# Performance work log

Measured on AMD Instinct MI355X. Metric: run time of the kernel, lower is better.

The kernel has to match this reference:

```python
import jax, jax.numpy as jnp
import numpy as np

L = 3          # num_layers
EPS = 1e-5     # BatchNorm eps


def _gmn_forward(feats_1, feats_2, edge_index_1, edge_index_2, N1, N2,
                 Wn, bn, Wm, bm, Wp, bp, gamma, beta, Wa, ba, Wg, bg, Wf, bf):
    N = N1 + N2
    x = jnp.concatenate([feats_1, feats_2], axis=0)                       # [N, F]
    edge_index = jnp.concatenate([edge_index_1, edge_index_2 + N1], axis=1)
    src, dst = edge_index[0], edge_index[1]                               # source_to_target flow
    batch = jnp.concatenate([jnp.zeros((N1,), jnp.int32), jnp.ones((N2,), jnp.int32)])
    for l in range(L):
        h = x @ Wn[l] + bn[l]                                             # lin_node
        # message(x_i=h[dst], x_j=h[src]) = lin_message(cat[x_i, x_j])
        m = jnp.concatenate([h[dst], h[src]], axis=1) @ Wm[l] + bm[l]     # [E, D]
        aggr = jax.ops.segment_sum(m, dst, num_segments=N)                # scatter-add to targets
        # batch_block_pair_attention on ORIGINAL (pre-lin_node) features
        gx, gy = x[:N1], x[N1:]
        s = gx @ gy.T                                                     # [N1, N2] similarities
        att_x = jax.nn.softmax(s, axis=1) @ gy                            # attn for graph-1 nodes
        att_y = jax.nn.softmax(s, axis=0).T @ gx                          # attn for graph-2 nodes
        cross = jnp.concatenate([att_x, att_y], axis=0)                   # [N, F]
        att_in = x - cross                                                # attention_input
        out = jnp.concatenate([aggr, att_in], axis=1) @ Wp[l] + bp[l]     # lin_passing
        mu = out.mean(axis=0)
        var = ((out - mu) ** 2).mean(axis=0)                              # BatchNorm (train, biased var)
        x = (out - mu) * jax.lax.rsqrt(var + EPS) * gamma[l] + beta[l]
    # GraphAggregator
    states = x @ Wa + ba
    gates = jax.nn.softmax(x @ Wg + bg, axis=1)                           # softmax over feature dim (as in source)
    g = states * gates
    sums = jax.ops.segment_sum(g, batch, num_segments=2)                  # scatter_mean
    counts = jnp.array([N1, N2], jnp.float32)[:, None]
    emb = (sums / counts) @ Wf + bf                                       # [2, D]
    return emb


def setup_inputs() -> dict:
    key = jax.random.key(0)
    ks = jax.random.split(key, 12)
    N1 = N2 = 6144
    E = 196608
    F = 128
    D = 128
    sc = lambda fan: fan ** -0.5
    rn = lambda k, sh, s: jax.random.normal(k, sh, dtype=jnp.float32) * s
    return {
        "feats_1": rn(ks[0], (N1, F), 1.0),
        "edge_index_1": jax.random.randint(ks[1], (2, E), 0, N1),
        "feats_2": rn(ks[2], (N2, F), 1.0),
        "edge_index_2": jax.random.randint(ks[3], (2, E), 0, N2),
        "sizes_1": N1,
        "sizes_2": N2,
        "Wn": rn(ks[4], (L, F, D), sc(F)),
        "bn": jnp.zeros((L, D), jnp.float32),
        "Wm": rn(ks[5], (L, 2 * D, D), sc(2 * D)),
        "bm": jnp.zeros((L, D), jnp.float32),
        "Wp": rn(ks[6], (L, D + F, D), sc(D + F)),
        "bp": jnp.zeros((L, D), jnp.float32),
        "gamma": jnp.ones((L, D), jnp.float32),
        "beta": jnp.zeros((L, D), jnp.float32),
        "Wa": rn(ks[7], (D, D), sc(D)),
        "ba": jnp.zeros((D,), jnp.float32),
        "Wg": rn(ks[8], (D, D), sc(D)),
        "bg": jnp.zeros((D,), jnp.float32),
        "Wf": rn(ks[9], (D, D), sc(D)),
        "bf": jnp.zeros((D,), jnp.float32),
    }


def reference(feats_1, edge_index_1, feats_2, edge_index_2, sizes_1, sizes_2,
              Wn, bn, Wm, bm, Wp, bp, gamma, beta, Wa, ba, Wg, bg, Wf, bf):
    emb = _gmn_forward(feats_1, feats_2, edge_index_1, edge_index_2,
                       int(sizes_1), int(sizes_2),
                       Wn, bn, Wm, bm, Wp, bp, gamma, beta, Wa, ba, Wg, bg, Wf, bf)
    emb_1 = emb[0:1]
    emb_2 = emb[1:2]
    return emb_1, emb_2
```

## Files before the change

kernel.cpp:

```cpp
#include <hip/hip_runtime.h>
#include <hip/hip_bf16.h>

#define D 128
#define KVS 16
typedef unsigned short u16;
typedef unsigned int u32;
typedef __attribute__((ext_vector_type(8))) short short8;
typedef __attribute__((ext_vector_type(16))) float f32x16;
typedef __attribute__((ext_vector_type(4))) u32 u32x4;

__device__ __forceinline__ u16 f2bf(float f){
  u32 u = __builtin_bit_cast(u32, f);
  u32 r = (u + 0x7FFFu + ((u >> 16) & 1u)) >> 16;
  return (u16)r;
}
__device__ __forceinline__ float bf2f(u16 u){
  union { u32 i; float f; } v; v.i = ((u32)u) << 16; return v.f;
}

__global__ void k_count(const int* __restrict__ ei1, const int* __restrict__ ei2,
                        int E1, int E2, int N1, int* __restrict__ cnt){
  int i = blockIdx.x*blockDim.x + threadIdx.x;
  int Et = E1 + E2;
  for (; i < Et; i += gridDim.x*blockDim.x){
    int dst = (i < E1) ? ei1[E1 + i] : (ei2[E2 + (i - E1)] + N1);
    atomicAdd(&cnt[dst], 1);
  }
}

__global__ void k_scan(const int* __restrict__ cnt, int* __restrict__ ptr,
                       int* __restrict__ cursor, float* __restrict__ degf, int N){
  __shared__ int part[256];
  int t = threadIdx.x;
  int per = (N + 255) >> 8;
  int lo = t*per, hi = min(N, lo+per);
  int s = 0;
  for (int j=lo;j<hi;j++) s += cnt[j];
  part[t] = s; __syncthreads();
  if (t==0){ int acc=0; for (int j=0;j<256;j++){ int v=part[j]; part[j]=acc; acc+=v; } }
  __syncthreads();
  int acc = part[t];
  for (int j=lo;j<hi;j++){ ptr[j]=acc; cursor[j]=acc; degf[j]=(float)cnt[j]; acc += cnt[j]; }
}

__global__ void k_fill(const int* __restrict__ ei1, const int* __restrict__ ei2,
                       int E1, int E2, int N1, int* __restrict__ cursor, int* __restrict__ srclist){
  int i = blockIdx.x*blockDim.x + threadIdx.x;
  int Et = E1 + E2;
  for (; i < Et; i += gridDim.x*blockDim.x){
    int src, dst;
    if (i < E1){ src = ei1[i]; dst = ei1[E1+i]; }
    else { int j = i - E1; src = ei2[j] + N1; dst = ei2[E2+j] + N1; }
    int p = atomicAdd(&cursor[dst], 1);
    srclist[p] = src;
  }
}

__global__ __launch_bounds__(256) void k_prep(
    const float* __restrict__ Wp, const float* __restrict__ Wa, const float* __restrict__ Wg,
    const float* __restrict__ Wn, const float* __restrict__ Wm,
    const float* __restrict__ bn, const float* __restrict__ bm,
    const float* __restrict__ src1, const float* __restrict__ src2, int N1,
    u16* __restrict__ wgt, u16* __restrict__ wfu, float* __restrict__ fbias,
    float* __restrict__ x, u16* __restrict__ xb, u16* __restrict__ xbT, int N)
{
  __shared__ u16 tile[128][136];
  const int m = blockIdx.x;
  const int t = threadIdx.x;
  if (m < 8){
    const float* src; u16* dst;
    if (m < 6){ int l = m % 3, half = m / 3; src = Wp + (size_t)l*32768 + half*16384; dst = wgt + (size_t)(half*3 + l)*16384; }
    else if (m == 6){ src = Wa; dst = wgt + (size_t)6*16384; }
    else { src = Wg; dst = wgt + (size_t)7*16384; }
    int n = t & 127, rh = t >> 7;
    for (int r0=0; r0<128; r0+=2){
      int r = r0 + rh;
      tile[n][r] = f2bf(src[r*128 + n]);
    }
    __syncthreads();
    int row = t >> 1, ch = t & 1;
    #pragma unroll
    for (int i=0;i<4;i++){
      int k0 = ch*64 + i*16;
      short8 a = *(const short8*)&tile[row][k0];
      short8 b = *(const short8*)&tile[row][k0+8];
      *(short8*)&dst[row*128 + k0] = a;
      *(short8*)&dst[row*128 + k0 + 8] = b;
    }
  } else if (m < 14){
    int blk = m - 8;
    int l = blk % 3, which = blk / 3;
    const float* A  = Wn + (size_t)l*16384;
    const float* Bm = Wm + (size_t)l*32768 + (which==0 ? 16384 : 0);
    u16* dst  = wfu  + (size_t)(which==0 ? l : 3+l)*16384;
    float* fb = fbias + (size_t)(which==0 ? l : 3+l)*128;
    int c0 = (t & 31) * 4;
    int r0 = (t >> 5) * 16;
    float acc[16][4];
    #pragma unroll
    for (int i=0;i<16;i++){ acc[i][0]=0.f; acc[i][1]=0.f; acc[i][2]=0.f; acc[i][3]=0.f; }
    for (int k=0;k<128;k++){
      float4 b4 = *(const float4*)&Bm[k*128 + c0];
      #pragma unroll
      for (int i=0;i<16;i++){
        float a = A[(r0+i)*128 + k];
        acc[i][0] += a*b4.x; acc[i][1] += a*b4.y; acc[i][2] += a*b4.z; acc[i][3] += a*b4.w;
      }
    }
    #pragma unroll
    for (int i=0;i<16;i++)
      #pragma unroll
      for (int j=0;j<4;j++)
        dst[(size_t)(c0+j)*128 + (r0+i)] = f2bf(acc[i][j]);
    if (t < 128){
      float s = 0.f;
      for (int k=0;k<128;k++) s += bn[l*128+k]*Bm[k*128+t];
      if (which) s += bm[l*128+t];
      fb[t] = s;
    }
  } else {
    int nb = (m - 14) * 128;
    int n = t >> 1, ch = t & 1;
    int row = nb + n;
    const float* srow = (row < N1) ? &src1[(size_t)row*D] : &src2[(size_t)(row-N1)*D];
    #pragma unroll
    for (int i=0;i<16;i++){
      int dd = ch*64 + i*4;
      float4 v = *(const float4*)&srow[dd];
      *(float4*)&x[(size_t)row*D + dd] = v;
      u16 b0 = f2bf(v.x), b1 = f2bf(v.y), b2 = f2bf(v.z), b3 = f2bf(v.w);
      ushort4 uv; uv.x=b0; uv.y=b1; uv.z=b2; uv.w=b3;
      *(ushort4*)&xb[(size_t)row*D + dd] = uv;
      tile[dd+0][n]=b0; tile[dd+1][n]=b1; tile[dd+2][n]=b2; tile[dd+3][n]=b3;
    }
    __syncthreads();
    int d = t & 127, hf = t >> 7;
    #pragma unroll
    for (int i=0;i<8;i++){
      short8 v = *(const short8*)&tile[d][hf*64 + i*8];
      *(short8*)&xbT[(size_t)d*N + nb + hf*64 + i*8] = v;
    }
  }
}

__global__ __launch_bounds__(256) void k_gemm(
    const u16* __restrict__ A, const u16* __restrict__ W1T,
    const u16* __restrict__ B, const u16* __restrict__ W2T,
    const float* __restrict__ bias, const float* __restrict__ bias2,
    const float* __restrict__ rs, const float* __restrict__ addin,
    float* __restrict__ of, float* __restrict__ of2,
    u16* __restrict__ ob, float* __restrict__ csums, int N)
{
  __shared__ __align__(16) u16 Wsw[2][16384];
  const int t = threadIdx.x;
  const int w4 = t >> 6;
  const int lane = t & 63;
  const int l31 = lane & 31;
  const int hi = lane >> 5;
  const int rb = blockIdx.x * 32;

  #pragma unroll
  for (int i=0;i<8;i++){
    int slot = i*256 + t;
    int row = slot >> 4, g = slot & 15;
    short8 v = *(const short8*)(W1T + row*128 + g*8);
    *(short8*)((char*)&Wsw[0][0] + row*256 + ((g ^ (row&7))*16)) = v;
  }
  if (B){
    #pragma unroll
    for (int i=0;i<8;i++){
      int slot = i*256 + t;
      int row = slot >> 4, g = slot & 15;
      short8 v = *(const short8*)(W2T + row*128 + g*8);
      *(short8*)((char*)&Wsw[1][0] + row*256 + ((g ^ (row&7))*16)) = v;
    }
  }
  short8 af[8], bfr[8];
  #pragma unroll
  for (int g=0; g<8; g++)
    af[g] = *(const short8*)(A + (size_t)(rb + l31)*D + (2*g + hi)*8);
  if (B){
    #pragma unroll
    for (int g=0; g<8; g++)
      bfr[g] = *(const short8*)(B + (size_t)(rb + l31)*D + (2*g + hi)*8);
  }
  __syncthreads();

  f32x16 acc1, acc2;
  #pragma unroll
  for (int i=0;i<16;i++){ acc1[i]=0.f; acc2[i]=0.f; }
  const int wrow = w4*32 + l31;
  #pragma unroll
  for (int s=0;s<8;s++){
    int gr = 2*s + hi;
    short8 wf = *(const short8*)((const char*)&Wsw[0][0] + wrow*256 + ((gr ^ (wrow&7))*16));
    acc1 = __builtin_amdgcn_mfma_f32_32x32x16_bf16(af[s], wf, acc1, 0,0,0);
  }
  if (B){
    #pragma unroll
    for (int s=0;s<8;s++){
      int gr = 2*s + hi;
      short8 wf = *(const short8*)((const char*)&Wsw[1][0] + wrow*256 + ((gr ^ (wrow&7))*16));
      acc2 = __builtin_amdgcn_mfma_f32_32x32x16_bf16(bfr[s], wf, acc2, 0,0,0);
    }
  }
  const int col = wrow;
  float bv = bias ? bias[col] : 0.0f;
  float bv2 = bias2 ? bias2[col] : 0.0f;
  float ssum = 0.f, sq = 0.f;
  #pragma unroll
  for (int r=0;r<16;r++){
    int rr = (r&3) + 8*(r>>2) + 4*hi;
    size_t grow = (size_t)(rb + rr);
    float v = acc1[r] + bv;
    if (rs) v *= rs[grow];
    if (addin) v += addin[grow*D + col];
    if (B && !of2) v += acc2[r];
    if (of) of[grow*D + col] = v;
    if (ob) ob[grow*D + col] = f2bf(v);
    if (of2) of2[grow*D + col] = acc2[r] + bv2;
    ssum += v; sq += v*v;
  }
  if (csums){
    ssum += __shfl_xor(ssum, 32, 64);
    sq   += __shfl_xor(sq, 32, 64);
    if (hi == 0){
      atomicAdd(&csums[col], ssum);
      atomicAdd(&csums[128+col], sq);
    }
  }
}

__global__ __launch_bounds__(256) void k_gather(const u16* __restrict__ hb, const int* __restrict__ ptr,
                          const int* __restrict__ cnt, const int* __restrict__ srclist,
                          float* __restrict__ Sg, int N){
  int f = threadIdx.x & 127, sub = threadIdx.x >> 7;
  int v = blockIdx.x*2 + sub;
  if (v >= N) return;
  int b = ptr[v], n = cnt[v];
  float a0=0.f, a1=0.f, a2=0.f, a3=0.f;
  int j=0;
  for (; j+3<n; j+=4){
    int s0=srclist[b+j], s1=srclist[b+j+1], s2=srclist[b+j+2], s3=srclist[b+j+3];
    a0 += bf2f(hb[(size_t)s0*D + f]);
    a1 += bf2f(hb[(size_t)s1*D + f]);
    a2 += bf2f(hb[(size_t)s2*D + f]);
    a3 += bf2f(hb[(size_t)s3*D + f]);
  }
  for (; j<n; j++) a0 += bf2f(hb[(size_t)srclist[b+j]*D + f]);
  Sg[(size_t)v*D + f] = (a0+a1)+(a2+a3);
}

__global__ __launch_bounds__(256, 2) void k_flash_mfma(
    const u16* __restrict__ xb, const u16* __restrict__ xbT,
    int N1, int N2, int Ntot,
    u16* __restrict__ Opartb, float* __restrict__ MLpart)
{
  __shared__ __align__(16) u16 Kbuf[2][4096];
  __shared__ __align__(16) u16 Vbuf[2][4096];

  const float L2E = 1.44269504f;
  const int t = threadIdx.x;
  const int w = t >> 6;
  const int lane = t & 63;
  const int l31 = lane & 31;
  const int hi = lane >> 5;

  const int qb = blockIdx.x / KVS;
  const int sp = blockIdx.x % KVS;
  const int qbase = qb * 128;
  const int qs = qbase + w*32;
  const bool isY = qbase >= N1;
  const int kv0 = isY ? 0 : N1;
  const int kvlen = isY ? N1 : N2;
  const int Lk = kvlen / KVS;
  const int kstart = kv0 + sp*Lk;
  const int ntiles = Lk >> 5;

  short8 qf[8];
  #pragma unroll
  for (int c = 0; c < 8; ++c)
    qf[c] = *(const short8*)(xb + (size_t)(qs + l31)*D + c*16 + hi*8);

  const int kr = t >> 3;
  const int kg = (t & 7) * 2;
  const int vd = t >> 1;
  const int vj = (t & 1) * 2;
  const int kw0 = kr*256 + ((kg     ^ (kr & 7))*16);
  const int kw1 = kr*256 + (((kg+1) ^ (kr & 7))*16);
  const int vw0 = vd*64  + (((vj     ^ vd) & 3)*16);
  const int vw1 = vd*64  + ((((vj+1) ^ vd) & 3)*16);

  f32x16 O[4];
  #pragma unroll
  for (int mt=0; mt<4; ++mt)
    #pragma unroll
    for (int i=0;i<16;i++) O[mt][i] = 0.f;
  float m_run = -3.0e38f, l_run = 0.0f;

  {
    int kb = kstart;
    short8 a0 = *(const short8*)(xb  + (size_t)(kb+kr)*D + kg*8);
    short8 a1 = *(const short8*)(xb  + (size_t)(kb+kr)*D + (kg+1)*8);
    short8 v0 = *(const short8*)(xbT + (size_t)vd*Ntot + kb + vj*8);
    short8 v1 = *(const short8*)(xbT + (size_t)vd*Ntot + kb + (vj+1)*8);
    *(short8*)((char*)&Kbuf[0][0] + kw0) = a0;
    *(short8*)((char*)&Kbuf[0][0] + kw1) = a1;
    *(short8*)((char*)&Vbuf[0][0] + vw0) = v0;
    *(short8*)((char*)&Vbuf[0][0] + vw1) = v1;
  }
  __syncthreads();

  for (int tt = 0; tt < ntiles; ++tt){
    const int cur = tt & 1;
    const int nxt = cur ^ 1;
    short8 a0, a1, v0, v1;
    const bool more = (tt+1 < ntiles);
    if (more){
      int kb = kstart + (tt+1)*32;
      a0 = *(const short8*)(xb  + (size_t)(kb+kr)*D + kg*8);
      a1 = *(const short8*)(xb  + (size_t)(kb+kr)*D + (kg+1)*8);
      v0 = *(const short8*)(xbT + (size_t)vd*Ntot + kb + vj*8);
      v1 = *(const short8*)(xbT + (size_t)vd*Ntot + kb + (vj+1)*8);
    }

    const char* Klds = (const char*)&Kbuf[cur][0];
    const char* Vlds = (const char*)&Vbuf[cur][0];

    f32x16 s;
    #pragma unroll
    for (int i=0;i<16;i++) s[i]=0.f;
    #pragma unroll
    for (int c = 0; c < 8; ++c){
      int gr = 2*c + hi;
      short8 ka = *(const short8*)(Klds + l31*256 + ((gr ^ (l31&7))*16));
      s = __builtin_amdgcn_mfma_f32_32x32x16_bf16(ka, qf[c], s, 0,0,0);
    }

    float tm = s[0];
    #pragma unroll
    for (int i=1;i<16;i++) tm = fmaxf(tm, s[i]);
    tm = fmaxf(tm, __shfl_xor(tm, 32, 64));
    float tm2 = tm * L2E;
    if (__any(tm2 > m_run + 11.544f)){
      float mnew = fmaxf(m_run, tm2);
      float alpha = exp2f(m_run - mnew);
      l_run *= alpha;
      m_run = mnew;
      #pragma unroll
      for (int i=0;i<16;i++){ O[0][i]*=alpha; O[1][i]*=alpha; O[2][i]*=alpha; O[3][i]*=alpha; }
    }
    float rsum = 0.f;
    #pragma unroll
    for (int i=0;i<16;i++){ float p = exp2f(fmaf(s[i], L2E, -m_run)); s[i]=p; rsum += p; }
    rsum += __shfl_xor(rsum, 32, 64);
    l_run += rsum;

    u32 pk[8];
    #pragma unroll
    for (int i=0;i<8;i++){
      u32 r;
      asm("v_cvt_pk_bf16_f32 %0, %1, %2" : "=v"(r) : "v"(s[2*i]), "v"(s[2*i+1]));
      pk[i] = r;
    }

    #pragma unroll
    for (int ks=0; ks<2; ++ks){
      u32 send0 = hi ? pk[(2*ks)*2+0] : pk[(2*ks+1)*2+0];
      u32 send1 = hi ? pk[(2*ks)*2+1] : pk[(2*ks+1)*2+1];
      u32 xv0 = (u32)__shfl_xor((int)send0, 32, 64);
      u32 xv1 = (u32)__shfl_xor((int)send1, 32, 64);
      u32 own0 = hi ? pk[(2*ks+1)*2+0] : pk[(2*ks)*2+0];
      u32 own1 = hi ? pk[(2*ks+1)*2+1] : pk[(2*ks)*2+1];
      u32x4 bv;
      bv.x = hi ? xv0 : own0;
      bv.y = hi ? xv1 : own1;
      bv.z = hi ? own0 : xv0;
      bv.w = hi ? own1 : xv1;
      short8 pf = __builtin_bit_cast(short8, bv);
      #pragma unroll
      for (int mt=0; mt<4; ++mt){
        int dd = mt*32 + l31;
        int j = 2*ks + hi;
        short8 vf = *(const short8*)(Vlds + dd*64 + (((j ^ dd) & 3)*16));
        O[mt] = __builtin_amdgcn_mfma_f32_32x32x16_bf16(vf, pf, O[mt], 0,0,0);
      }
    }

    if (more){
      *(short8*)((char*)&Kbuf[nxt][0] + kw0) = a0;
      *(short8*)((char*)&Kbuf[nxt][0] + kw1) = a1;
      *(short8*)((char*)&Vbuf[nxt][0] + vw0) = v0;
      *(short8*)((char*)&Vbuf[nxt][0] + vw1) = v1;
    }
    __syncthreads();
  }

  const int strip = qs >> 5;
  u16* Od = Opartb + ((size_t)strip*KVS + sp)*4096;
  #pragma unroll
  for (int mt=0; mt<4; ++mt){
    #pragma unroll
    for (int r=0;r<16;r++){
      int dd = mt*32 + (r&3) + 8*(r>>2) + 4*hi;
      Od[dd*32 + l31] = f2bf(O[mt][r]);
    }
  }
  if (lane < 32){
    float* mlp = MLpart + ((size_t)strip*KVS + sp)*64;
    mlp[l31*2+0] = m_run;
    mlp[l31*2+1] = l_run;
  }
}

__global__ __launch_bounds__(256) void k_fcomb_hm2(
    const u16* __restrict__ Opartb, const float* __restrict__ MLpart,
    const float* __restrict__ x, u16* __restrict__ attinb,
    const u16* __restrict__ xb, const u16* __restrict__ W1T, const float* __restrict__ fb2,
    u16* __restrict__ hm2b, int nstrips, int N)
{
  __shared__ __align__(16) char smem[32768];
  const int t = threadIdx.x;
  if ((int)blockIdx.x < nstrips){
    const int strip = blockIdx.x;
    float (*cw)[32] = (float(*)[32])smem;
    float (*Tld)[33] = (float(*)[33])(smem + 2048);
    if (t < 32){
      const float* mlp = MLpart + (size_t)strip*KVS*64;
      float mv[KVS], lv[KVS];
      float M = -3.0e38f;
      #pragma unroll
      for (int s2=0;s2<KVS;s2++){ mv[s2]=mlp[s2*64+t*2]; lv[s2]=mlp[s2*64+t*2+1]; M = fmaxf(M, mv[s2]); }
      float L = 0.f;
      #pragma unroll
      for (int s2=0;s2<KVS;s2++){ float wv=exp2f(mv[s2]-M); cw[s2][t]=wv; L += wv*lv[s2]; }
      float inv = 1.0f / L;
      #pragma unroll
      for (int s2=0;s2<KVS;s2++) cw[s2][t] *= inv;
    }
    __syncthreads();
    {
      const int d = t >> 1, q0 = (t & 1) * 16;
      const u16* Ob = Opartb + (size_t)strip*KVS*4096;
      float acc[16];
      #pragma unroll
      for (int j=0;j<16;j++) acc[j]=0.f;
      #pragma unroll
      for (int s2=0; s2<KVS; ++s2){
        const u16* row = Ob + s2*4096 + d*32 + q0;
        short8 v8a = *(const short8*)row;
        short8 v8b = *(const short8*)(row + 8);
        #pragma unroll
        for (int j=0;j<8;j++){
          acc[j]   += cw[s2][q0+j]  *bf2f((u16)v8a[j]);
          acc[8+j] += cw[s2][q0+8+j]*bf2f((u16)v8b[j]);
        }
      }
      #pragma unroll
      for (int j=0;j<16;j++) Tld[d][q0+j] = acc[j];
    }
    __syncthreads();
    {
      const int q = t >> 3, c0 = (t & 7) * 16;
      const size_t row = (size_t)(strip*32 + q)*D;
      #pragma unroll
      for (int i=0;i<16;i+=4){
        float4 xr = *(const float4*)&x[row + c0 + i];
        ushort4 o;
        o.x = f2bf(xr.x - Tld[c0+i+0][q]);
        o.y = f2bf(xr.y - Tld[c0+i+1][q]);
        o.z = f2bf(xr.z - Tld[c0+i+2][q]);
        o.w = f2bf(xr.w - Tld[c0+i+3][q]);
        *(ushort4*)&attinb[row + c0 + i] = o;
      }
    }
  } else {
    u16* Wsw = (u16*)smem;
    const int w4 = t >> 6;
    const int lane = t & 63;
    const int l31 = lane & 31;
    const int hi = lane >> 5;
    const int rb = ((int)blockIdx.x - nstrips) * 32;
    #pragma unroll
    for (int i=0;i<8;i++){
      int slot = i*256 + t;
      int row = slot >> 4, g = slot & 15;
      short8 v = *(const short8*)(W1T + row*128 + g*8);
      *(short8*)((char*)Wsw + row*256 + ((g ^ (row&7))*16)) = v;
    }
    short8 af[8];
    #pragma unroll
    for (int g=0; g<8; g++)
      af[g] = *(const short8*)(xb + (size_t)(rb + l31)*D + (2*g + hi)*8);
    __syncthreads();
    f32x16 acc1;
    #pragma unroll
    for (int i=0;i<16;i++) acc1[i]=0.f;
    const int wrow = w4*32 + l31;
    #pragma unroll
    for (int s=0;s<8;s++){
      int gr = 2*s + hi;
      short8 wf = *(const short8*)((const char*)Wsw + wrow*256 + ((gr ^ (wrow&7))*16));
      acc1 = __builtin_amdgcn_mfma_f32_32x32x16_bf16(af[s], wf, acc1, 0,0,0);
    }
    float bv = fb2[wrow];
    #pragma unroll
    for (int r=0;r<16;r++){
      int rr = (r&3) + 8*(r>>2) + 4*hi;
      hm2b[(size_t)(rb + rr)*D + wrow] = f2bf(acc1[r] + bv);
    }
  }
}

__global__ __launch_bounds__(256) void k_normcvt(const float* __restrict__ outb,
                        const float* __restrict__ sums,
                        const float* __restrict__ gamma, const float* __restrict__ beta,
                        int N, float* __restrict__ x, u16* __restrict__ xb, u16* __restrict__ xbT){
  __shared__ u16 tile[128][136];
  __shared__ float smu[128], srs[128], sg2[128], sb2[128];
  int t = threadIdx.x;
  if (t < 128){
    float mu = sums[t] / (float)N;
    float var = fmaxf(sums[128+t]/(float)N - mu*mu, 0.0f);
    smu[t]=mu; srs[t]=rsqrtf(var + 1e-5f);
    sg2[t]=gamma[t]; sb2[t]=beta[t];
  }
  __syncthreads();
  int nb = blockIdx.x * 128;
  int n = t >> 1, ch = t & 1;
  #pragma unroll
  for (int i=0;i<16;i++){
    int dd = ch*64 + i*4;
    float4 v = *(const float4*)&outb[(size_t)(nb+n)*D + dd];
    float4 y;
    y.x = (v.x - smu[dd+0])*srs[dd+0]*sg2[dd+0] + sb2[dd+0];
    y.y = (v.y - smu[dd+1])*srs[dd+1]*sg2[dd+1] + sb2[dd+1];
    y.z = (v.z - smu[dd+2])*srs[dd+2]*sg2[dd+2] + sb2[dd+2];
    y.w = (v.w - smu[dd+3])*srs[dd+3]*sg2[dd+3] + sb2[dd+3];
    *(float4*)&x[(size_t)(nb+n)*D + dd] = y;
    u16 b0=f2bf(y.x), b1=f2bf(y.y), b2=f2bf(y.z), b3=f2bf(y.w);
    ushort4 uv; uv.x=b0; uv.y=b1; uv.z=b2; uv.w=b3;
    *(ushort4*)&xb[(size_t)(nb+n)*D + dd] = uv;
    tile[dd+0][n]=b0; tile[dd+1][n]=b1; tile[dd+2][n]=b2; tile[dd+3][n]=b3;
  }
  __syncthreads();
  int d = t & 127, hf = t >> 7;
  #pragma unroll
  for (int i=0;i<8;i++){
    short8 v = *(const short8*)&tile[d][hf*64 + i*8];
    *(short8*)&xbT[(size_t)d*N + nb + hf*64 + i*8] = v;
  }
}

__global__ __launch_bounds__(256) void k_gatepool(
    const float* __restrict__ states, const float* __restrict__ glog,
    int N1, int N, float* __restrict__ gsums)
{
  __shared__ float part[256];
  part[threadIdx.x] = 0.f;
  __syncthreads();
  int wid = threadIdx.x >> 6, lane = threadIdx.x & 63;
  for (int v = blockIdx.x*4 + wid; v < N; v += gridDim.x*4){
    float a0 = glog[(size_t)v*D + lane], a1 = glog[(size_t)v*D + lane + 64];
    float mx = fmaxf(a0,a1);
    #pragma unroll
    for (int off=32; off; off>>=1) mx = fmaxf(mx, __shfl_xor(mx, off, 64));
    float e0 = __expf(a0-mx), e1 = __expf(a1-mx);
    float ss = e0+e1;
    #pragma unroll
    for (int off=32; off; off>>=1) ss += __shfl_xor(ss, off, 64);
    float inv = 1.f/ss;
    int g = (v < N1) ? 0 : 1;
    atomicAdd(&part[g*128 + lane], states[(size_t)v*D+lane]*e0*inv);
    atomicAdd(&part[g*128 + lane + 64], states[(size_t)v*D+lane+64]*e1*inv);
  }
  __syncthreads();
  atomicAdd(&gsums[threadIdx.x], part[threadIdx.x]);
}

__global__ __launch_bounds__(256) void k_emb(
    const float* __restrict__ gsums, const float* __restrict__ Wf,
    const float* __restrict__ bf_, int N1, int N2, float* __restrict__ outp)
{
  __shared__ float mean[256];
  int t = threadIdx.x;
  mean[t] = gsums[t] / ((t < 128) ? (float)N1 : (float)N2);
  __syncthreads();
  int g = t >> 7, dc = t & 127;
  float acc = bf_[dc];
  for (int k=0;k<D;k++) acc += mean[g*128 + k] * Wf[k*D + dc];
  outp[t] = acc;
}

extern "C" void kernel_launch(void* const* d_in, const int* in_sizes, int n_in,
                              void* d_out, int out_size, void* d_ws, size_t ws_size,
                              hipStream_t stream) {
  const float* feats1 = (const float*)d_in[0];
  const int*   ei1    = (const int*)d_in[1];
  const float* feats2 = (const float*)d_in[2];
  const int*   ei2    = (const int*)d_in[3];
  const float* Wn = (const float*)d_in[6];
  const float* bn = (const float*)d_in[7];
  const float* Wm = (const float*)d_in[8];
  const float* bm = (const float*)d_in[9];
  const float* Wp = (const float*)d_in[10];
  const float* bp = (const float*)d_in[11];
  const float* gamma = (const float*)d_in[12];
  const float* beta  = (const float*)d_in[13];
  const float* Wa = (const float*)d_in[14];
  const float* ba = (const float*)d_in[15];
  const float* Wg = (const float*)d_in[16];
  const float* bg = (const float*)d_in[17];
  const float* Wf = (const float*)d_in[18];
  const float* bff = (const float*)d_in[19];

  int N1 = in_sizes[0]/D, E1 = in_sizes[1]/2;
  int N2 = in_sizes[2]/D, E2 = in_sizes[3]/2;
  int N = N1+N2;
  int nstrips = N/32;

  char* w = (char*)d_ws;
  float* x    = (float*)w; w += (size_t)N*D*4;
  u16* xb     = (u16*)w;   w += (size_t)N*D*2;
  u16* xbT    = (u16*)w;   w += (size_t)N*D*2;
  u16* hm2b   = (u16*)w;   w += (size_t)N*D*2;
  u16* aggrb  = (u16*)w;   w += (size_t)N*D*2;
  u16* attinb = (u16*)w;   w += (size_t)N*D*2;
  int* cnt    = (int*)w;   w += (size_t)N*4;
  float* sums = (float*)w; w += 3*256*4;
  float* gsums= (float*)w; w += 256*4;
  int* ptr    = (int*)w;   w += (size_t)N*4;
  int* cursor = (int*)w;   w += (size_t)N*4;
  float* degf = (float*)w; w += (size_t)N*4;
  int* srclist= (int*)w;   w += (size_t)(E1+E2)*4;
  u16* wgt    = (u16*)w;   w += (size_t)8*16384*2;
  u16* wfu    = (u16*)w;   w += (size_t)6*16384*2;
  float* fbias= (float*)w; w += (size_t)6*128*4;
  u16* Opartb = (u16*)w;   w += (size_t)nstrips*KVS*4096*2;
  float* MLpart=(float*)w; w += (size_t)nstrips*KVS*64*4;
  float* Sg     = (float*)Opartb;
  float* outb   = (float*)Opartb + (size_t)N*D;
  float* states = Sg;
  float* glog   = outb;

  hipMemsetAsync(cnt, 0, (size_t)N*4 + 4*256*4, stream);
  k_count<<<1024,256,0,stream>>>(ei1, ei2, E1, E2, N1, cnt);
  k_scan<<<1,256,0,stream>>>(cnt, ptr, cursor, degf, N);
  k_fill<<<1024,256,0,stream>>>(ei1, ei2, E1, E2, N1, cursor, srclist);
  k_prep<<<14 + N/128,256,0,stream>>>(Wp, Wa, Wg, Wn, Wm, bn, bm,
                                      feats1, feats2, N1, wgt, wfu, fbias, x, xb, xbT, N);

  for (int l=0;l<3;l++){
    const u16* fuse2T_l = wfu + (size_t)l*16384;
    const u16* fuse1T_l = wfu + (size_t)(3+l)*16384;
    const float* fb2_l  = fbias + (size_t)l*128;
    const float* fb1_l  = fbias + (size_t)(3+l)*128;
    const u16* Wp1T_l = wgt + (size_t)(0+l)*16384;
    const u16* Wp2T_l = wgt + (size_t)(3+l)*16384;
    const float* bp_l = bp + (size_t)l*D;
    float* sums_l = sums + (size_t)l*256;

    k_flash_mfma<<<(N/128)*KVS,256,0,stream>>>(xb, xbT, N1, N2, N, Opartb, MLpart);
    k_fcomb_hm2<<<nstrips + N/32,256,0,stream>>>(Opartb, MLpart, x, attinb,
                                                 xb, fuse2T_l, fb2_l, hm2b, nstrips, N);
    k_gather<<<N/2,256,0,stream>>>(hm2b, ptr, cnt, srclist, Sg, N);
    k_gemm<<<N/32,256,0,stream>>>(xb, fuse1T_l, nullptr, nullptr, fb1_l, nullptr,
                                  degf, Sg, nullptr, nullptr, aggrb, nullptr, N);
    k_gemm<<<N/32,256,0,stream>>>(aggrb, Wp1T_l, attinb, Wp2T_l, bp_l, nullptr,
                                  nullptr, nullptr, outb, nullptr, nullptr, sums_l, N);
    k_normcvt<<<N/128,256,0,stream>>>(outb, sums_l, gamma + (size_t)l*D, beta + (size_t)l*D, N, x, xb, xbT);
  }

  k_gemm<<<N/32,256,0,stream>>>(xb, wgt + (size_t)6*16384, xb, wgt + (size_t)7*16384,
                                ba, bg, nullptr, nullptr, states, glog, nullptr, nullptr, N);
  k_gatepool<<<64,256,0,stream>>>(states, glog, N1, N, gsums);
  k_emb<<<1,256,0,stream>>>(gsums, Wf, bff, N1, N2, (float*)d_out);
}
```

Before: 634.6 us.

## Gather raw neighbor features before projection and merge into dual-input aggregation GEMM

The edge aggregation now sums neighbor bf16 features x_src directly, instead of first projecting every node through the fused Wn·Wm2 weight and then gathering. The source-side projection is folded into the aggregation k_gemm as a second A/B operand pair. This removes the per-node hm2 MFMA path from the combine kernel, and the two fused biases are merged into one degree-scaled bias. The weight-prep kernel also stages A through LDS as bf16. In exchange, neighbor sums are rounded to bf16 before the matmul, which may add precision error.

```diff
diff --git a/kernel.cpp b/kernel.cpp
--- a/kernel.cpp
+++ b/kernel.cpp
@@ -93,7 +93,19 @@
     const float* A  = Wn + (size_t)l*16384;
     const float* Bm = Wm + (size_t)l*32768 + (which==0 ? 16384 : 0);
     u16* dst  = wfu  + (size_t)(which==0 ? l : 3+l)*16384;
-    float* fb = fbias + (size_t)(which==0 ? l : 3+l)*128;
+    {
+      int r = t >> 1, kh = t & 1;
+      #pragma unroll
+      for (int i=0;i<16;i++){
+        int k0 = kh*64 + i*4;
+        float4 v4 = *(const float4*)&A[r*128 + k0];
+        tile[k0+0][r] = f2bf(v4.x);
+        tile[k0+1][r] = f2bf(v4.y);
+        tile[k0+2][r] = f2bf(v4.z);
+        tile[k0+3][r] = f2bf(v4.w);
+      }
+    }
+    __syncthreads();
     int c0 = (t & 31) * 4;
     int r0 = (t >> 5) * 16;
     float acc[16][4];
@@ -101,10 +113,17 @@
     for (int i=0;i<16;i++){ acc[i][0]=0.f; acc[i][1]=0.f; acc[i][2]=0.f; acc[i][3]=0.f; }
     for (int k=0;k<128;k++){
       float4 b4 = *(const float4*)&Bm[k*128 + c0];
+      short8 a0 = *(const short8*)&tile[k][r0];
+      short8 a1 = *(const short8*)&tile[k][r0+8];
       #pragma unroll
-      for (int i=0;i<16;i++){
-        float a = A[(r0+i)*128 + k];
-        acc[i][0] += a*b4.x; acc[i][1] += a*b4.y; acc[i][2] += a*b4.z; acc[i][3] += a*b4.w;
+      for (int i=0;i<8;i++){
+        float fa = bf2f((u16)a0[i]);
+        acc[i][0] += fa*b4.x; acc[i][1] += fa*b4.y; acc[i][2] += fa*b4.z; acc[i][3] += fa*b4.w;
+      }
+      #pragma unroll
+      for (int i=0;i<8;i++){
+        float fa = bf2f((u16)a1[i]);
+        acc[8+i][0] += fa*b4.x; acc[8+i][1] += fa*b4.y; acc[8+i][2] += fa*b4.z; acc[8+i][3] += fa*b4.w;
       }
     }
     #pragma unroll
@@ -112,11 +131,12 @@
       #pragma unroll
       for (int j=0;j<4;j++)
         dst[(size_t)(c0+j)*128 + (r0+i)] = f2bf(acc[i][j]);
-    if (t < 128){
+    if (which == 1 && t < 128){
+      const float* Bm1 = Wm + (size_t)l*32768;
+      const float* Bm2 = Bm1 + 16384;
       float s = 0.f;
-      for (int k=0;k<128;k++) s += bn[l*128+k]*Bm[k*128+t];
-      if (which) s += bm[l*128+t];
-      fb[t] = s;
+      for (int k=0;k<128;k++) s += bn[l*128+k]*(Bm1[k*128+t] + Bm2[k*128+t]);
+      fbias[l*128+t] = s + bm[l*128+t];
     }
   } else {
     int nb = (m - 14) * 128;
@@ -233,7 +253,7 @@
 
 __global__ __launch_bounds__(256) void k_gather(const u16* __restrict__ hb, const int* __restrict__ ptr,
                           const int* __restrict__ cnt, const int* __restrict__ srclist,
-                          float* __restrict__ Sg, int N){
+                          u16* __restrict__ xgb, int N){
   int f = threadIdx.x & 127, sub = threadIdx.x >> 7;
   int v = blockIdx.x*2 + sub;
   if (v >= N) return;
@@ -248,7 +268,7 @@
     a3 += bf2f(hb[(size_t)s3*D + f]);
   }
   for (; j<n; j++) a0 += bf2f(hb[(size_t)srclist[b+j]*D + f]);
-  Sg[(size_t)v*D + f] = (a0+a1)+(a2+a3);
+  xgb[(size_t)v*D + f] = f2bf((a0+a1)+(a2+a3));
 }
 
 __global__ __launch_bounds__(256, 2) void k_flash_mfma(
@@ -413,101 +433,61 @@
   }
 }
 
-__global__ __launch_bounds__(256) void k_fcomb_hm2(
+__global__ __launch_bounds__(256) void k_fcomb(
     const u16* __restrict__ Opartb, const float* __restrict__ MLpart,
-    const float* __restrict__ x, u16* __restrict__ attinb,
-    const u16* __restrict__ xb, const u16* __restrict__ W1T, const float* __restrict__ fb2,
-    u16* __restrict__ hm2b, int nstrips, int N)
+    const float* __restrict__ x, u16* __restrict__ attinb)
 {
-  __shared__ __align__(16) char smem[32768];
+  __shared__ float cw[KVS][32];
+  __shared__ float Tld[128][33];
+  const int strip = blockIdx.x;
   const int t = threadIdx.x;
-  if ((int)blockIdx.x < nstrips){
-    const int strip = blockIdx.x;
-    float (*cw)[32] = (float(*)[32])smem;
-    float (*Tld)[33] = (float(*)[33])(smem + 2048);
-    if (t < 32){
-      const float* mlp = MLpart + (size_t)strip*KVS*64;
-      float mv[KVS], lv[KVS];
-      float M = -3.0e38f;
+  if (t < 32){
+    const float* mlp = MLpart + (size_t)strip*KVS*64;
+    float mv[KVS], lv[KVS];
+    float M = -3.0e38f;
+    #pragma unroll
+    for (int s2=0;s2<KVS;s2++){ mv[s2]=mlp[s2*64+t*2]; lv[s2]=mlp[s2*64+t*2+1]; M = fmaxf(M, mv[s2]); }
+    float L = 0.f;
+    #pragma unroll
+    for (int s2=0;s2<KVS;s2++){ float wv=exp2f(mv[s2]-M); cw[s2][t]=wv; L += wv*lv[s2]; }
+    float inv = 1.0f / L;
+    #pragma unroll
+    for (int s2=0;s2<KVS;s2++) cw[s2][t] *= inv;
+  }
+  __syncthreads();
+  {
+    const int d = t >> 1, q0 = (t & 1) * 16;
+    const u16* Ob = Opartb + (size_t)strip*KVS*4096;
+    float acc[16];
+    #pragma unroll
+    for (int j=0;j<16;j++) acc[j]=0.f;
+    #pragma unroll
+    for (int s2=0; s2<KVS; ++s2){
+      const u16* row = Ob + s2*4096 + d*32 + q0;
+      short8 v8a = *(const short8*)row;
+      short8 v8b = *(const short8*)(row + 8);
       #pragma unroll
-      for (int s2=0;s2<KVS;s2++){ mv[s2]=mlp[s2*64+t*2]; lv[s2]=mlp[s2*64+t*2+1]; M = fmaxf(M, mv[s2]); }
-      float L = 0.f;
-      #pragma unroll
-      for (int s2=0;s2<KVS;s2++){ float wv=exp2f(mv[s2]-M); cw[s2][t]=wv; L += wv*lv[s2]; }
-      float inv = 1.0f / L;
-      #pragma unroll
-      for (int s2=0;s2<KVS;s2++) cw[s2][t] *= inv;
-    }
-    __syncthreads();
-    {
-      const int d = t >> 1, q0 = (t & 1) * 16;
-      const u16* Ob = Opartb + (size_t)strip*KVS*4096;
-      float acc[16];
-      #pragma unroll
-      for (int j=0;j<16;j++) acc[j]=0.f;
-      #pragma unroll
-      for (int s2=0; s2<KVS; ++s2){
-        const u16* row = Ob + s2*4096 + d*32 + q0;
-        short8 v8a = *(const short8*)row;
-        short8 v8b = *(const short8*)(row + 8);
-        #pragma unroll
-        for (int j=0;j<8;j++){
-          acc[j]   += cw[s2][q0+j]  *bf2f((u16)v8a[j]);
-          acc[8+j] += cw[s2][q0+8+j]*bf2f((u16)v8b[j]);
-        }
+      for (int j=0;j<8;j++){
+        acc[j]   += cw[s2][q0+j]  *bf2f((u16)v8a[j]);
+        acc[8+j] += cw[s2][q0+8+j]*bf2f((u16)v8b[j]);
       }
-      #pragma unroll
-      for (int j=0;j<16;j++) Tld[d][q0+j] = acc[j];
-    }
-    __syncthreads();
-    {
-      const int q = t >> 3, c0 = (t & 7) * 16;
-      const size_t row = (size_t)(strip*32 + q)*D;
-      #pragma unroll
-      for (int i=0;i<16;i+=4){
-        float4 xr = *(const float4*)&x[row + c0 + i];
-        ushort4 o;
-        o.x = f2bf(xr.x - Tld[c0+i+0][q]);
-        o.y = f2bf(xr.y - Tld[c0+i+1][q]);
-        o.z = f2bf(xr.z - Tld[c0+i+2][q]);
-        o.w = f2bf(xr.w - Tld[c0+i+3][q]);
-        *(ushort4*)&attinb[row + c0 + i] = o;
-      }
-    }
-  } else {
-    u16* Wsw = (u16*)smem;
-    const int w4 = t >> 6;
-    const int lane = t & 63;
-    const int l31 = lane & 31;
-    const int hi = lane >> 5;
-    const int rb = ((int)blockIdx.x - nstrips) * 32;
-    #pragma unroll
-    for (int i=0;i<8;i++){
-      int slot = i*256 + t;
-      int row = slot >> 4, g = slot & 15;
-      short8 v = *(const short8*)(W1T + row*128 + g*8);
-      *(short8*)((char*)Wsw + row*256 + ((g ^ (row&7))*16)) = v;
-    }
-    short8 af[8];
-    #pragma unroll
-    for (int g=0; g<8; g++)
-      af[g] = *(const short8*)(xb + (size_t)(rb + l31)*D + (2*g + hi)*8);
-    __syncthreads();
-    f32x16 acc1;
-    #pragma unroll
-    for (int i=0;i<16;i++) acc1[i]=0.f;
-    const int wrow = w4*32 + l31;
-    #pragma unroll
-    for (int s=0;s<8;s++){
-      int gr = 2*s + hi;
-      short8 wf = *(const short8*)((const char*)Wsw + wrow*256 + ((gr ^ (wrow&7))*16));
-      acc1 = __builtin_amdgcn_mfma_f32_32x32x16_bf16(af[s], wf, acc1, 0,0,0);
-    }
-    float bv = fb2[wrow];
-    #pragma unroll
-    for (int r=0;r<16;r++){
-      int rr = (r&3) + 8*(r>>2) + 4*hi;
-      hm2b[(size_t)(rb + rr)*D + wrow] = f2bf(acc1[r] + bv);
+    }
+    #pragma unroll
+    for (int j=0;j<16;j++) Tld[d][q0+j] = acc[j];
+  }
+  __syncthreads();
+  {
+    const int q = t >> 3, c0 = (t & 7) * 16;
+    const size_t row = (size_t)(strip*32 + q)*D;
+    #pragma unroll
+    for (int i=0;i<16;i+=4){
+      float4 xr = *(const float4*)&x[row + c0 + i];
+      ushort4 o;
+      o.x = f2bf(xr.x - Tld[c0+i+0][q]);
+      o.y = f2bf(xr.y - Tld[c0+i+1][q]);
+      o.z = f2bf(xr.z - Tld[c0+i+2][q]);
+      o.w = f2bf(xr.w - Tld[c0+i+3][q]);
+      *(ushort4*)&attinb[row + c0 + i] = o;
     }
   }
 }
@@ -623,7 +603,7 @@
   float* x    = (float*)w; w += (size_t)N*D*4;
   u16* xb     = (u16*)w;   w += (size_t)N*D*2;
   u16* xbT    = (u16*)w;   w += (size_t)N*D*2;
-  u16* hm2b   = (u16*)w;   w += (size_t)N*D*2;
+  u16* xgb    = (u16*)w;   w += (size_t)N*D*2;
   u16* aggrb  = (u16*)w;   w += (size_t)N*D*2;
   u16* attinb = (u16*)w;   w += (size_t)N*D*2;
   int* cnt    = (int*)w;   w += (size_t)N*4;
@@ -635,12 +615,11 @@
   int* srclist= (int*)w;   w += (size_t)(E1+E2)*4;
   u16* wgt    = (u16*)w;   w += (size_t)8*16384*2;
   u16* wfu    = (u16*)w;   w += (size_t)6*16384*2;
-  float* fbias= (float*)w; w += (size_t)6*128*4;
+  float* fbias= (float*)w; w += (size_t)3*128*4;
   u16* Opartb = (u16*)w;   w += (size_t)nstrips*KVS*4096*2;
   float* MLpart=(float*)w; w += (size_t)nstrips*KVS*64*4;
-  float* Sg     = (float*)Opartb;
   float* outb   = (float*)Opartb + (size_t)N*D;
-  float* states = Sg;
+  float* states = (float*)Opartb;
   float* glog   = outb;
 
   hipMemsetAsync(cnt, 0, (size_t)N*4 + 4*256*4, stream);
@@ -653,19 +632,17 @@
   for (int l=0;l<3;l++){
     const u16* fuse2T_l = wfu + (size_t)l*16384;
     const u16* fuse1T_l = wfu + (size_t)(3+l)*16384;
-    const float* fb2_l  = fbias + (size_t)l*128;
-    const float* fb1_l  = fbias + (size_t)(3+l)*128;
+    const float* fb_l   = fbias + (size_t)l*128;
     const u16* Wp1T_l = wgt + (size_t)(0+l)*16384;
     const u16* Wp2T_l = wgt + (size_t)(3+l)*16384;
     const float* bp_l = bp + (size_t)l*D;
     float* sums_l = sums + (size_t)l*256;
 
     k_flash_mfma<<<(N/128)*KVS,256,0,stream>>>(xb, xbT, N1, N2, N, Opartb, MLpart);
-    k_fcomb_hm2<<<nstrips + N/32,256,0,stream>>>(Opartb, MLpart, x, attinb,
-                                                 xb, fuse2T_l, fb2_l, hm2b, nstrips, N);
-    k_gather<<<N/2,256,0,stream>>>(hm2b, ptr, cnt, srclist, Sg, N);
-    k_gemm<<<N/32,256,0,stream>>>(xb, fuse1T_l, nullptr, nullptr, fb1_l, nullptr,
-                                  degf, Sg, nullptr, nullptr, aggrb, nullptr, N);
+    k_fcomb<<<nstrips,256,0,stream>>>(Opartb, MLpart, x, attinb);
+    k_gather<<<N/2,256,0,stream>>>(xb, ptr, cnt, srclist, xgb, N);
+    k_gemm<<<N/32,256,0,stream>>>(xb, fuse1T_l, xgb, fuse2T_l, fb_l, nullptr,
+                                  degf, nullptr, nullptr, nullptr, aggrb, nullptr, N);
     k_gemm<<<N/32,256,0,stream>>>(aggrb, Wp1T_l, attinb, Wp2T_l, bp_l, nullptr,
                                   nullptr, nullptr, outb, nullptr, nullptr, sums_l, N);
     k_normcvt<<<N/128,256,0,stream>>>(outb, sums_l, gamma + (size_t)l*D, beta + (size_t)l*D, N, x, xb, xbT);
```

New measurement: 604.0 us. 1.05x faster.
